# Optimization experiments

Hardware: AMD Instinct MI355X
Metric: run time of the kernel (lower is better)

The kernel has to match this reference:

```python
import jax, jax.numpy as jnp
import numpy as np

N, E, K, C, NB, G = 10000, 320000, 10, 32, 8, 8
RMAX, AVG = 5.0, 32.0
L_OF_M = np.array([0,1,1,1,2,2,2,2,2,3,3,3,3,3,3,3])
BLOCKS = [(0,1),(1,4),(4,9),(9,16)]


def _sph(u):
    # real spherical harmonics l=0..3, e3nn 'component' normalization (sum_m Y_lm^2 = 2l+1)
    x, y, z = u[:,0], u[:,1], u[:,2]
    s3=3**0.5; s5=5**0.5; s15=15**0.5; s105=105**0.5
    s35_8=(35.0/8.0)**0.5; s21_8=(21.0/8.0)**0.5; s7=7**0.5
    return jnp.stack([
        jnp.ones_like(x),
        s3*x, s3*y, s3*z,
        s15*x*y, s15*y*z, 0.5*s5*(3*z*z-1.0), s15*x*z, 0.5*s15*(x*x-y*y),
        s35_8*y*(3*x*x-y*y), s105*x*y*z, s21_8*y*(5*z*z-1.0),
        0.5*s7*z*(5*z*z-3.0), s21_8*x*(5*z*z-1.0), 0.5*s105*z*(x*x-y*y),
        s35_8*x*(x*x-3*y*y)], axis=-1)


def _radial(r):
    # Bessel basis * polynomial cutoff (p=5)
    n = jnp.arange(1, NB+1, dtype=r.dtype)
    bess = jnp.sqrt(2.0/RMAX)*jnp.sin(n*jnp.pi*r[:,None]/RMAX)/r[:,None]
    t = r/RMAX; p = 5.0
    env = 1.0 - (p+1)*(p+2)/2*t**5 + p*(p+2)*t**6 - p*(p+1)/2*t**7
    env = jnp.where(r < RMAX, env, 0.0)
    return bess*env[:,None]


def _interact(scal, ea, ef, snd, rcv, mws, Wl, n_nodes):
    h = ef
    for W in mws[:-1]:
        h = jax.nn.silu(h @ W)
    tw = (h @ mws[-1]).reshape(-1, C, 4)[:, :, L_OF_M]          # [E,C,16] per-(channel,l) tp weights
    mji = scal[snd][:, :, None] * tw * ea[:, None, :]            # per-edge CG-style tensor product
    msg = jax.ops.segment_sum(mji, rcv, num_segments=n_nodes) / AVG
    return jnp.concatenate([jnp.einsum('ncm,cd->ndm', msg[:, :, a:b], Wl[l])
                            for l, (a, b) in enumerate(BLOCKS)], axis=-1)


def _forward(positions, node_attrs, shifts, edge_index, batch, num_graphs,
             atomic_energies, W_emb, Wup1, M1a, M1b, M1c, M1d, Wl1, Wprod1,
             Wup2, M2a, M2b, M2c, M2d, Wl2, Wprod2, Wsc2, wr1, Wr2a, wr2b):
    snd, rcv = edge_index[0], edge_index[1]
    vec = positions[rcv] - positions[snd] + shifts
    r = jnp.sqrt(jnp.sum(vec*vec, -1) + 1e-12)
    ea = _sph(vec / r[:, None])           # [E,16]
    ef = _radial(r)                       # [E,8]
    nf0 = node_attrs @ W_emb              # node embedding [N,C]
    A1 = _interact(nf0 @ Wup1, ea, ef, snd, rcv, (M1a, M1b, M1c, M1d), Wl1, positions.shape[0])
    c1 = jnp.einsum('nk,kct->nct', node_attrs, Wprod1)          # element-dep product-basis coeffs
    a0 = A1[:, :, 0]
    nf1 = A1 * (c1[..., 0] + c1[..., 1]*a0 + c1[..., 2]*a0*a0)[:, :, None]  # correlation-3 product
    A2 = _interact(nf1[:, :, 0] @ Wup2, ea, ef, snd, rcv, (M2a, M2b, M2c, M2d), Wl2, positions.shape[0])
    pl = jnp.stack([jnp.sum(A2[:, :, a:b]**2, -1) for a, b in BLOCKS], -1)  # [N,C,4] invariants
    c2 = jnp.einsum('nk,kct->nct', node_attrs, Wprod2)
    nf2 = jnp.sum(c2*pl, -1) + jnp.einsum('nk,nc,kcd->nd', node_attrs, nf1[:, :, 0], Wsc2)
    e0 = node_attrs @ atomic_energies
    e1 = nf1[:, :, 0] @ wr1
    e2 = jax.nn.silu(nf2 @ Wr2a) @ wr2b
    node_energy = e0 + e1 + e2
    total = jax.ops.segment_sum(node_energy, batch, num_segments=num_graphs)
    return total, node_energy


def setup_inputs():
    key = jax.random.key(0)
    ks = jax.random.split(key, 24)
    s = 0.1
    inp = {}
    inp['positions'] = jax.random.normal(ks[0], (N, 3), jnp.float32)
    inp['node_attrs'] = jax.nn.one_hot(jax.random.randint(ks[1], (N,), 0, K), K, dtype=jnp.float32)
    inp['shifts'] = jnp.zeros((E, 3), jnp.float32)
    inp['edge_index'] = jax.random.randint(ks[2], (2, E), 0, N)
    inp['batch'] = jnp.sort(jax.random.randint(ks[3], (N,), 0, G))
    inp['num_graphs'] = G
    inp['atomic_energies'] = jax.random.normal(ks[4], (K,), jnp.float32)
    inp['W_emb'] = s*jax.random.normal(ks[5], (K, C), jnp.float32)
    inp['Wup1'] = s*jax.random.normal(ks[6], (C, C), jnp.float32)
    inp['M1a'] = s*jax.random.normal(ks[7], (NB, 64), jnp.float32)
    inp['M1b'] = s*jax.random.normal(ks[8], (64, 64), jnp.float32)
    inp['M1c'] = s*jax.random.normal(ks[9], (64, 64), jnp.float32)
    inp['M1d'] = s*jax.random.normal(ks[10], (64, C*4), jnp.float32)
    inp['Wl1'] = s*jax.random.normal(ks[11], (4, C, C), jnp.float32)
    inp['Wprod1'] = s*jax.random.normal(ks[12], (K, C, 3), jnp.float32)
    inp['Wup2'] = s*jax.random.normal(ks[13], (C, C), jnp.float32)
    inp['M2a'] = s*jax.random.normal(ks[14], (NB, 64), jnp.float32)
    inp['M2b'] = s*jax.random.normal(ks[15], (64, 64), jnp.float32)
    inp['M2c'] = s*jax.random.normal(ks[16], (64, 64), jnp.float32)
    inp['M2d'] = s*jax.random.normal(ks[17], (64, C*4), jnp.float32)
    inp['Wl2'] = s*jax.random.normal(ks[18], (4, C, C), jnp.float32)
    inp['Wprod2'] = s*jax.random.normal(ks[19], (K, C, 4), jnp.float32)
    inp['Wsc2'] = s*jax.random.normal(ks[20], (K, C, C), jnp.float32)
    inp['wr1'] = s*jax.random.normal(ks[21], (C,), jnp.float32)
    inp['Wr2a'] = s*jax.random.normal(ks[22], (C, 16), jnp.float32)
    inp['wr2b'] = s*jax.random.normal(ks[23], (16,), jnp.float32)
    return inp


def reference(positions, node_attrs, shifts, edge_index, batch, num_graphs,
              atomic_energies, W_emb, Wup1, M1a, M1b, M1c, M1d, Wl1, Wprod1,
              Wup2, M2a, M2b, M2c, M2d, Wl2, Wprod2, Wsc2, wr1, Wr2a, wr2b):
    def efn(pos):
        tot, ne = _forward(pos, node_attrs, shifts, edge_index, batch, num_graphs,
                           atomic_energies, W_emb, Wup1, M1a, M1b, M1c, M1d, Wl1, Wprod1,
                           Wup2, M2a, M2b, M2c, M2d, Wl2, Wprod2, Wsc2, wr1, Wr2a, wr2b)
        return jnp.sum(tot), (tot, ne)
    (_, (total, node_energy)), g = jax.value_and_grad(efn, has_aux=True)(positions)
    forces = -g  # forces = -dE/dpositions as in get_outputs
    return total, node_energy, forces
```

## Files before the change

### kernel.cpp

```cpp
#include <hip/hip_runtime.h>
#include <math.h>

#define NN 10000
#define NE 320000
#define KS 10
#define CC 32
#define GG 8
#define NTAB 2048
#define TROW 320
#define RMAXf 5.0f
#define AVGf 32.0f

#define OF_TAB 0
#define SZ_TAB ((NTAB + 1) * TROW)
#define OF_GEO (OF_TAB + SZ_TAB)
#define OF_SND (OF_GEO + 4 * NE)
#define OF_SPK (OF_SND + NE)
#define OF_RCSR (OF_SPK + NE)
#define OF_SC1 (OF_RCSR + NE)
#define OF_SP (OF_SC1 + KS * CC)
#define OF_RE (OF_SP + NN)
#define OF_UE (OF_RE + NE)
#define OF_GV (OF_UE + 3 * NE)
#define OF_A0 (OF_GV + 3 * NE)
#define OF_NF1 (OF_A0 + NN * CC)
#define OF_SCAL2 (OF_NF1 + NN * CC)
#define OF_NEP (OF_SCAL2 + NN * CC)
#define OF_GM2T (OF_NEP + NN)
#define OF_GNF1P (OF_GM2T + NN * CC * 16)
#define OF_GS1 (OF_GNF1P + NN * CC)
#define OF_ROWS (OF_GS1 + NN * CC)
#define OF_ELIST (OF_ROWS + NN + 1)
#define OF_DEG (OF_ELIST + NE)
#define OF_CUR (OF_DEG + NN)
#define OF_GSC2 (OF_CUR + NN)
#define OF_END (OF_GSC2 + NN * CC)

__device__ __forceinline__ int lm_of(int m) { return (m == 0) ? 0 : (m < 4) ? 1 : (m < 9) ? 2 : 3; }

__device__ __forceinline__ void sph16(float x, float y, float z, float* Y) {
    const float s3 = 1.7320508075688772f, s5 = 2.23606797749979f, s15 = 3.872983346207417f,
                s105 = 10.246950765959598f, s358 = 2.091650066335189f,
                s218 = 1.6201851746019651f, s7 = 2.6457513110645907f;
    Y[0] = 1.f;
    Y[1] = s3 * x; Y[2] = s3 * y; Y[3] = s3 * z;
    Y[4] = s15 * x * y; Y[5] = s15 * y * z; Y[6] = 0.5f * s5 * (3.f * z * z - 1.f);
    Y[7] = s15 * x * z; Y[8] = 0.5f * s15 * (x * x - y * y);
    Y[9] = s358 * y * (3.f * x * x - y * y);
    Y[10] = s105 * x * y * z;
    Y[11] = s218 * y * (5.f * z * z - 1.f);
    Y[12] = 0.5f * s7 * z * (5.f * z * z - 3.f);
    Y[13] = s218 * x * (5.f * z * z - 1.f);
    Y[14] = 0.5f * s105 * z * (x * x - y * y);
    Y[15] = s358 * x * (x * x - 3.f * y * y);
}

__device__ __forceinline__ void sph16_grad(float x, float y, float z, float* Dx, float* Dy, float* Dz) {
    const float s3 = 1.7320508075688772f, s5 = 2.23606797749979f, s15 = 3.872983346207417f,
                s105 = 10.246950765959598f, s358 = 2.091650066335189f,
                s218 = 1.6201851746019651f, s7 = 2.6457513110645907f;
    Dx[0] = 0; Dy[0] = 0; Dz[0] = 0;
    Dx[1] = s3; Dy[1] = 0; Dz[1] = 0;
    Dx[2] = 0; Dy[2] = s3; Dz[2] = 0;
    Dx[3] = 0; Dy[3] = 0; Dz[3] = s3;
    Dx[4] = s15 * y; Dy[4] = s15 * x; Dz[4] = 0;
    Dx[5] = 0; Dy[5] = s15 * z; Dz[5] = s15 * y;
    Dx[6] = 0; Dy[6] = 0; Dz[6] = 3.f * s5 * z;
    Dx[7] = s15 * z; Dy[7] = 0; Dz[7] = s15 * x;
    Dx[8] = s15 * x; Dy[8] = -s15 * y; Dz[8] = 0;
    Dx[9] = 6.f * s358 * x * y; Dy[9] = 3.f * s358 * (x * x - y * y); Dz[9] = 0;
    Dx[10] = s105 * y * z; Dy[10] = s105 * x * z; Dz[10] = s105 * x * y;
    Dx[11] = 0; Dy[11] = s218 * (5.f * z * z - 1.f); Dz[11] = 10.f * s218 * y * z;
    Dx[12] = 0; Dy[12] = 0; Dz[12] = 0.5f * s7 * (15.f * z * z - 3.f);
    Dx[13] = s218 * (5.f * z * z - 1.f); Dy[13] = 0; Dz[13] = 10.f * s218 * x * z;
    Dx[14] = s105 * x * z; Dy[14] = -s105 * y * z; Dz[14] = 0.5f * s105 * (x * x - y * y);
    Dx[15] = 3.f * s358 * (x * x - y * y); Dy[15] = -6.f * s358 * x * y; Dz[15] = 0;
}

__global__ void k_species(const float* __restrict__ na, int* __restrict__ sp) {
    int n = blockIdx.x * blockDim.x + threadIdx.x;
    if (n >= NN) return;
    int k = 0;
    for (int j = 0; j < KS; j++)
        if (na[n * KS + j] > 0.5f) k = j;
    sp[n] = k;
}

__global__ void k_scal1(const float* __restrict__ Wemb, const float* __restrict__ Wup1, float* __restrict__ st) {
    int i = threadIdx.x;
    if (i >= KS * CC) return;
    int k = i / CC, c = i % CC;
    float s = 0;
    for (int j = 0; j < CC; j++) s += Wemb[k * CC + j] * Wup1[j * CC + c];
    st[i] = s;
}

__global__ void k_table(const float* __restrict__ M1a, const float* __restrict__ M1b,
                        const float* __restrict__ M1c, const float* __restrict__ M1d,
                        const float* __restrict__ M2a, const float* __restrict__ M2b,
                        const float* __restrict__ M2c, const float* __restrict__ M2d,
                        float* __restrict__ tab) {
    const double PI = 3.14159265358979323846;
    int row = blockIdx.x;
    int j = threadIdx.x;
    __shared__ float sR[8], sdR[8];
    __shared__ float sA[64], sdA[64], sB[64], sdB[64];
    if (j < 8) {
        double r = (double)row * ((double)RMAXf / NTAB);
        if (r < 1e-6) r = 1e-6;
        double a = (double)(j + 1) * PI / (double)RMAXf;
        double env = 0.0, denv = 0.0;
        if (row < NTAB) {
            double t = r / (double)RMAXf;
            double t4 = t * t * t * t;
            env = 1.0 - 21.0 * t4 * t + 35.0 * t4 * t * t - 15.0 * t4 * t * t * t;
            denv = (-105.0 * t4 + 210.0 * t4 * t - 105.0 * t4 * t * t) / (double)RMAXf;
        }
        double pref = sqrt(2.0 / (double)RMAXf);
        double s = sin(a * r), cg = cos(a * r);
        double bess = pref * s / r;
        double dbess = pref * (a * cg / r - s / (r * r));
        sR[j] = (float)(bess * env);
        sdR[j] = (float)(dbess * env + bess * denv);
    }
    __syncthreads();
    size_t rb = (size_t)row * TROW;

    {
        float p = 0, dp = 0;
        for (int i = 0; i < 8; i++) { float w = M1a[i * 64 + j]; p += sR[i] * w; dp += sdR[i] * w; }
        float sg = 1.f / (1.f + expf(-p));
        sB[j] = p * sg; sdB[j] = dp * sg * (1.f + p * (1.f - sg));
    }
    __syncthreads();
    {
        float p = 0, dp = 0;
        for (int i = 0; i < 64; i++) { float w = M1b[i * 64 + j]; p += sB[i] * w; dp += sdB[i] * w; }
        float sg = 1.f / (1.f + expf(-p));
        sA[j] = p * sg; sdA[j] = dp * sg * (1.f + p * (1.f - sg));
    }
    __syncthreads();
    {
        float p = 0, dp = 0;
        for (int i = 0; i < 64; i++) { float w = M1c[i * 64 + j]; p += sA[i] * w; dp += sdA[i] * w; }
        float sg = 1.f / (1.f + expf(-p));
        sB[j] = p * sg; sdB[j] = dp * sg * (1.f + p * (1.f - sg));
    }
    __syncthreads();
    #pragma unroll
    for (int t2 = 0; t2 < 2; t2++) {
        int o = j + t2 * 64;
        if ((o & 3) == 0) {
            float p = 0, dp = 0;
            for (int i = 0; i < 64; i++) { float w = M1d[i * 128 + o]; p += sB[i] * w; dp += sdB[i] * w; }
            int c = o >> 2;
            tab[rb + c] = p;
            tab[rb + 32 + c] = dp;
        }
    }
    __syncthreads();

    {
        float p = 0, dp = 0;
        for (int i = 0; i < 8; i++) { float w = M2a[i * 64 + j]; p += sR[i] * w; dp += sdR[i] * w; }
        float sg = 1.f / (1.f + expf(-p));
        sB[j] = p * sg; sdB[j] = dp * sg * (1.f + p * (1.f - sg));
    }
    __syncthreads();
    {
        float p = 0, dp = 0;
        for (int i = 0; i < 64; i++) { float w = M2b[i * 64 + j]; p += sB[i] * w; dp += sdB[i] * w; }
        float sg = 1.f / (1.f + expf(-p));
        sA[j] = p * sg; sdA[j] = dp * sg * (1.f + p * (1.f - sg));
    }
    __syncthreads();
    {
        float p = 0, dp = 0;
        for (int i = 0; i < 64; i++) { float w = M2c[i * 64 + j]; p += sA[i] * w; dp += sdA[i] * w; }
        float sg = 1.f / (1.f + expf(-p));
        sB[j] = p * sg; sdB[j] = dp * sg * (1.f + p * (1.f - sg));
    }
    __syncthreads();
    #pragma unroll
    for (int t2 = 0; t2 < 2; t2++) {
        int o = j + t2 * 64;
        float p = 0, dp = 0;
        for (int i = 0; i < 64; i++) { float w = M2d[i * 128 + o]; p += sB[i] * w; dp += sdB[i] * w; }
        tab[rb + 64 + o] = p;
        tab[rb + 192 + o] = dp;
    }
}

__global__ void k_geom(const float* __restrict__ pos, const float* __restrict__ shifts,
                       const int* __restrict__ ei, float* __restrict__ re,
                       float* __restrict__ ue, int* __restrict__ deg) {
    int e = blockIdx.x * 256 + threadIdx.x;
    if (e >= NE) return;
    int s = ei[e], t = ei[NE + e];
    float vx = pos[3 * t] - pos[3 * s] + shifts[3 * e];
    float vy = pos[3 * t + 1] - pos[3 * s + 1] + shifts[3 * e + 1];
    float vz = pos[3 * t + 2] - pos[3 * s + 2] + shifts[3 * e + 2];
    float r = sqrtf(vx * vx + vy * vy + vz * vz + 1e-12f);
    float inv = 1.f / r;
    re[e] = r;
    ue[3 * e] = vx * inv;
    ue[3 * e + 1] = vy * inv;
    ue[3 * e + 2] = vz * inv;
    atomicAdd(&deg[t], 1);
}

__global__ void k_scan(const int* __restrict__ deg, int* __restrict__ rows, int* __restrict__ cur) {
    __shared__ int part[1024];
    int t = threadIdx.x;
    const int per = (NN + 1023) / 1024;
    int base = t * per;
    int s = 0;
    for (int i = 0; i < per; i++) {
        int idx = base + i;
        if (idx < NN) s += deg[idx];
    }
    part[t] = s;
    __syncthreads();
    for (int off = 1; off < 1024; off <<= 1) {
        int v = (t >= off) ? part[t - off] : 0;
        __syncthreads();
        part[t] += v;
        __syncthreads();
    }
    int run = (t == 0) ? 0 : part[t - 1];
    for (int i = 0; i < per; i++) {
        int idx = base + i;
        if (idx < NN) {
            rows[idx] = run;
            cur[idx] = run;
            run += deg[idx];
        }
    }
    if (t == 1023) rows[NN] = run;
}

__global__ void k_fill(const int* __restrict__ ei, const int* __restrict__ sp,
                       const float* __restrict__ re, const float* __restrict__ ue,
                       int* __restrict__ cur, int* __restrict__ elist,
                       int* __restrict__ snd, int* __restrict__ spk,
                       float* __restrict__ rcsr, float4* __restrict__ geo) {
    int e = blockIdx.x * 256 + threadIdx.x;
    if (e >= NE) return;
    int s = ei[e], t = ei[NE + e];
    int p = atomicAdd(&cur[t], 1);
    elist[p] = e;
    snd[p] = s;
    spk[p] = sp[s];
    rcsr[p] = re[e];
    geo[p] = make_float4(re[e], ue[3 * e], ue[3 * e + 1], ue[3 * e + 2]);
}

__global__ __launch_bounds__(256, 4)
void k_gather1(const int* __restrict__ rows, const int* __restrict__ spk,
               const float* __restrict__ rcsr, const int* __restrict__ sp,
               const float* __restrict__ sc1, const float* __restrict__ tab,
               const float* __restrict__ Wl1, const float* __restrict__ Wprod1,
               const float* __restrict__ Wup2, const float* __restrict__ wr1,
               const float* __restrict__ aE,
               float* __restrict__ a0s, float* __restrict__ nf1,
               float* __restrict__ scal2, float* __restrict__ nep) {
    int wid = (blockIdx.x * 256 + threadIdx.x) >> 6;
    int lane = threadIdx.x & 63, c = lane & 31, h = lane >> 5, hb = h << 5;
    if (wid >= NN) return;
    int r0 = rows[wid], dg = rows[wid + 1] - r0;
    float acc = 0.f;
    for (int j = h; j < dg; j += 2) {
        int p = r0 + j;
        float r = rcsr[p];
        int kk = spk[p];
        float w1 = 0.f;
        if (r < RMAXf) {
            float tt = r * (NTAB / RMAXf);
            int i = (int)tt; if (i > NTAB - 1) i = NTAB - 1;
            float f = tt - (float)i;
            size_t b = (size_t)i * TROW + c;
            w1 = tab[b] * (1.f - f) + tab[b + TROW] * f;
        }
        acc += sc1[kk * CC + c] * w1;
    }
    acc += __shfl_xor(acc, 32, 64);
    float a0 = 0.f;
    for (int d = 0; d < CC; d++) a0 += __shfl(acc, hb + d, 64) * Wl1[d * CC + c];
    a0 *= (1.f / AVGf);
    int k = sp[wid];
    const float* cp = &Wprod1[(k * CC + c) * 3];
    float nf = a0 * (cp[0] + cp[1] * a0 + cp[2] * a0 * a0);
    float s2 = 0.f;
    for (int d = 0; d < CC; d++) s2 += __shfl(nf, hb + d, 64) * Wup2[d * CC + c];
    float t1 = nf * wr1[c];
    for (int m = 16; m >= 1; m >>= 1) t1 += __shfl_xor(t1, m, 64);
    if (h == 0) {
        a0s[wid * CC + c] = a0;
        nf1[wid * CC + c] = nf;
        scal2[wid * CC + c] = s2;
        if (c == 0) nep[wid] = aE[k] + t1;
    }
}

__global__ __launch_bounds__(256, 4)
void k_node2(const int* __restrict__ rows, const int* __restrict__ snd,
             const float4* __restrict__ geo, const int* __restrict__ sp,
             const float* __restrict__ scal2, const float* __restrict__ tab,
             const float* __restrict__ Wl2, const float* __restrict__ Wprod2,
             const float* __restrict__ Wsc2, const float* __restrict__ nf1,
             const float* __restrict__ Wr2a, const float* __restrict__ wr2b,
             const float* __restrict__ wr1, const float* __restrict__ nep,
             const int* __restrict__ batch,
             float* __restrict__ gm2T, float* __restrict__ gnf1p,
             float* __restrict__ out_total, float* __restrict__ out_ne) {
    __shared__ float lds[4][16 * 32];
    int wid = (blockIdx.x * 256 + threadIdx.x) >> 6;
    int lane = threadIdx.x & 63, c = lane & 31, h = lane >> 5, hb = h << 5;
    int w = threadIdx.x >> 6;
    if (wid >= NN) return;
    int r0 = rows[wid], dg = rows[wid + 1] - r0;
    float S2r[16];
    #pragma unroll
    for (int m = 0; m < 16; m++) S2r[m] = 0.f;
    for (int j = h; j < dg; j += 2) {
        int p = r0 + j;
        float4 g4 = geo[p];
        int s = snd[p];
        float sc = scal2[s * CC + c];
        float r = g4.x;
        float w2[4] = {0, 0, 0, 0};
        if (r < RMAXf) {
            float tt = r * (NTAB / RMAXf);
            int i = (int)tt; if (i > NTAB - 1) i = NTAB - 1;
            float f = tt - (float)i;
            size_t b = (size_t)i * TROW + 64 + c * 4;
            #pragma unroll
            for (int l = 0; l < 4; l++) w2[l] = tab[b + l] * (1.f - f) + tab[b + TROW + l] * f;
        }
        float Y[16];
        sph16(g4.y, g4.z, g4.w, Y);
        #pragma unroll
        for (int m = 0; m < 16; m++) S2r[m] += sc * w2[lm_of(m)] * Y[m];
    }
    #pragma unroll
    for (int m = 0; m < 16; m++) S2r[m] += __shfl_xor(S2r[m], 32, 64);
    if (h == 0) {
        #pragma unroll
        for (int m = 0; m < 16; m++) lds[w][m * 32 + c] = S2r[m];
    }
    __syncthreads();
    int d = c;
    float A2r[16];
    #pragma unroll
    for (int m = 0; m < 16; m++) {
        const float* wl = &Wl2[lm_of(m) * CC * CC];
        float acc = 0;
        for (int cc = 0; cc < CC; cc++) acc += lds[w][m * 32 + cc] * wl[cc * CC + d];
        A2r[m] = acc * (1.f / AVGf);
    }
    float pl[4] = {0, 0, 0, 0};
    #pragma unroll
    for (int m = 0; m < 16; m++) pl[lm_of(m)] += A2r[m] * A2r[m];
    int k = sp[wid];
    const float* c2 = &Wprod2[(k * CC + d) * 4];
    float nf2 = c2[0] * pl[0] + c2[1] * pl[1] + c2[2] * pl[2] + c2[3] * pl[3];
    for (int cc = 0; cc < CC; cc++) nf2 += nf1[wid * CC + cc] * Wsc2[((size_t)k * CC + cc) * CC + d];
    int jj = d & 15;
    float zj = 0;
    for (int dd = 0; dd < CC; dd++) zj += __shfl(nf2, hb + dd, 64) * Wr2a[dd * 16 + jj];
    float sg = 1.f / (1.f + expf(-zj));
    float e2p = (d < 16) ? zj * sg * wr2b[jj] : 0.f;
    float red = e2p;
    for (int m = 16; m >= 1; m >>= 1) red += __shfl_xor(red, m, 64);
    if (h == 0 && d == 0) {
        float ne = nep[wid] + red;
        out_ne[wid] = ne;
        atomicAdd(&out_total[batch[wid]], ne);
    }
    float gz = sg * (1.f + zj * (1.f - sg)) * wr2b[jj];
    float gn = 0;
    for (int j2 = 0; j2 < 16; j2++) gn += Wr2a[d * 16 + j2] * __shfl(gz, hb + j2, 64);
    __syncthreads();
    if (h == 0) {
        #pragma unroll
        for (int m = 0; m < 16; m++) lds[w][m * 32 + d] = 2.f * A2r[m] * gn * c2[lm_of(m)];
    }
    __syncthreads();
    float gmv[16];
    #pragma unroll
    for (int m = 0; m < 16; m++) {
        const float* wl = &Wl2[lm_of(m) * CC * CC + c * CC];
        float acc = 0;
        for (int dd = 0; dd < CC; dd++) acc += lds[w][m * 32 + dd] * wl[dd];
        gmv[m] = acc * (1.f / AVGf);
    }
    float g1 = wr1[c];
    for (int dd = 0; dd < CC; dd++) g1 += __shfl(gn, hb + dd, 64) * Wsc2[((size_t)k * CC + c) * CC + dd];
    if (h == 0) {
        #pragma unroll
        for (int m = 0; m < 16; m++) gm2T[(size_t)wid * 512 + c * 16 + m] = gmv[m];
        gnf1p[wid * CC + c] = g1;
    }
}

__global__ __launch_bounds__(256, 4)
void k_gbwd2(const int* __restrict__ rows, const int* __restrict__ elist,
             const int* __restrict__ snd, const float4* __restrict__ geo,
             const float* __restrict__ scal2, const float* __restrict__ tab,
             const float* __restrict__ gm2T,
             float* __restrict__ gsc2, float* __restrict__ gvec) {
    int wid = (blockIdx.x * 256 + threadIdx.x) >> 6;
    int lane = threadIdx.x & 63, c = lane & 31, h = lane >> 5;
    if (wid >= NN) return;
    float gm[16];
    #pragma unroll
    for (int m = 0; m < 16; m++) gm[m] = gm2T[(size_t)wid * 512 + c * 16 + m];
    int r0 = rows[wid], dg = rows[wid + 1] - r0;
    for (int j = h; j < dg; j += 2) {
        int p = r0 + j;
        float4 g4 = geo[p];
        int s = snd[p];
        float sc = scal2[s * CC + c];
        float r = g4.x, ux = g4.y, uy = g4.z, uz = g4.w;
        float w2[4] = {0, 0, 0, 0}, dw2[4] = {0, 0, 0, 0};
        if (r < RMAXf) {
            float tt = r * (NTAB / RMAXf);
            int i = (int)tt; if (i > NTAB - 1) i = NTAB - 1;
            float f = tt - (float)i;
            size_t b = (size_t)i * TROW + 64 + c * 4;
            size_t b2 = (size_t)i * TROW + 192 + c * 4;
            #pragma unroll
            for (int l = 0; l < 4; l++) {
                w2[l] = tab[b + l] * (1.f - f) + tab[b + TROW + l] * f;
                dw2[l] = tab[b2 + l] * (1.f - f) + tab[b2 + TROW + l] * f;
            }
        }
        float Y[16], Dx[16], Dy[16], Dz[16];
        sph16(ux, uy, uz, Y);
        sph16_grad(ux, uy, uz, Dx, Dy, Dz);
        float gsc = 0, gdr = 0, gx = 0, gy = 0, gz = 0;
        #pragma unroll
        for (int m = 0; m < 16; m++) {
            float g = gm[m];
            int l = lm_of(m);
            float wv = w2[l];
            gsc += g * wv * Y[m];
            gdr += g * Y[m] * sc * dw2[l];
            float gY = g * sc * wv;
            gx += gY * Dx[m]; gy += gY * Dy[m]; gz += gY * Dz[m];
        }
        atomicAdd(&gsc2[s * CC + c], gsc);
        for (int m2 = 16; m2 >= 1; m2 >>= 1) {
            gdr += __shfl_xor(gdr, m2, 64);
            gx += __shfl_xor(gx, m2, 64);
            gy += __shfl_xor(gy, m2, 64);
            gz += __shfl_xor(gz, m2, 64);
        }
        if (c == 0) {
            int e = elist[p];
            float inv = 1.f / r;
            float dot = ux * gx + uy * gy + uz * gz;
            gvec[3 * e] = ux * gdr + (gx - ux * dot) * inv;
            gvec[3 * e + 1] = uy * gdr + (gy - uy * dot) * inv;
            gvec[3 * e + 2] = uz * gdr + (gz - uz * dot) * inv;
        }
    }
}

__global__ void k_node_bwd2(const float* __restrict__ gnf1p, const float* __restrict__ gsc2,
                            const float* __restrict__ Wup2, const float* __restrict__ a0s,
                            const int* __restrict__ sp, const float* __restrict__ Wprod1,
                            const float* __restrict__ Wl1, float* __restrict__ gS1) {
    int gid = blockIdx.x * 256 + threadIdx.x;
    int n = gid >> 5, c = gid & 31;
    if (n >= NN) return;
    int hb = threadIdx.x & 32;
    float g1 = gnf1p[n * CC + c];
    for (int dd = 0; dd < CC; dd++) g1 += gsc2[n * CC + dd] * Wup2[c * CC + dd];
    float a0 = a0s[n * CC + c];
    int k = sp[n];
    const float* cp = &Wprod1[(k * CC + c) * 3];
    float ga0 = g1 * (cp[0] + 2.f * cp[1] * a0 + 3.f * cp[2] * a0 * a0);
    float acc = 0;
    for (int dd = 0; dd < CC; dd++) acc += __shfl(ga0, hb + dd, 64) * Wl1[c * CC + dd];
    gS1[n * CC + c] = acc * (1.f / AVGf);
}

__global__ void k_edge_bwd1(const int* __restrict__ ei, const int* __restrict__ sp,
                            const float* __restrict__ re, const float* __restrict__ ue,
                            const float* __restrict__ sc1, const float* __restrict__ tab,
                            const float* __restrict__ gS1, const float* __restrict__ gvec,
                            float* __restrict__ F) {
    int gid = blockIdx.x * 256 + threadIdx.x;
    int e = gid >> 5, c = gid & 31;
    if (e >= NE) return;
    int s = ei[e], t = ei[NE + e];
    float r = re[e];
    float dw = 0.f;
    if (r < RMAXf) {
        float tt = r * (NTAB / RMAXf);
        int i = (int)tt; if (i > NTAB - 1) i = NTAB - 1;
        float f = tt - (float)i;
        size_t b = (size_t)i * TROW + 32 + c;
        dw = tab[b] * (1.f - f) + tab[b + TROW] * f;
    }
    float gw = gS1[t * CC + c] * sc1[sp[s] * CC + c];
    float gdr = gw * dw;
    for (int m = 16; m >= 1; m >>= 1) gdr += __shfl_xor(gdr, m, 64);
    if (c < 3) {
        float u = ue[3 * e + c];
        float gv = gvec[3 * e + c] + u * gdr;
        atomicAdd(&F[3 * s + c], gv);
        atomicAdd(&F[3 * t + c], -gv);
    }
}

extern "C" void kernel_launch(void* const* d_in, const int* in_sizes, int n_in,
                              void* d_out, int out_size, void* d_ws, size_t ws_size,
                              hipStream_t stream) {
    const float* pos = (const float*)d_in[0];
    const float* na = (const float*)d_in[1];
    const float* shifts = (const float*)d_in[2];
    const int* ei = (const int*)d_in[3];
    const int* batch = (const int*)d_in[4];
    const float* aE = (const float*)d_in[6];
    const float* Wemb = (const float*)d_in[7];
    const float* Wup1 = (const float*)d_in[8];
    const float* M1a = (const float*)d_in[9];
    const float* M1b = (const float*)d_in[10];
    const float* M1c = (const float*)d_in[11];
    const float* M1d = (const float*)d_in[12];
    const float* Wl1 = (const float*)d_in[13];
    const float* Wprod1 = (const float*)d_in[14];
    const float* Wup2 = (const float*)d_in[15];
    const float* M2a = (const float*)d_in[16];
    const float* M2b = (const float*)d_in[17];
    const float* M2c = (const float*)d_in[18];
    const float* M2d = (const float*)d_in[19];
    const float* Wl2 = (const float*)d_in[20];
    const float* Wprod2 = (const float*)d_in[21];
    const float* Wsc2 = (const float*)d_in[22];
    const float* wr1 = (const float*)d_in[23];
    const float* Wr2a = (const float*)d_in[24];
    const float* wr2b = (const float*)d_in[25];

    float* ws = (float*)d_ws;
    float* tab = ws + OF_TAB;
    float4* geo = (float4*)(ws + OF_GEO);
    int* snd = (int*)(ws + OF_SND);
    int* spk = (int*)(ws + OF_SPK);
    float* rcsr = ws + OF_RCSR;
    float* sc1 = ws + OF_SC1;
    int* sp = (int*)(ws + OF_SP);
    float* re = ws + OF_RE;
    float* ue = ws + OF_UE;
    float* gv = ws + OF_GV;
    float* a0s = ws + OF_A0;
    float* nf1 = ws + OF_NF1;
    float* scal2 = ws + OF_SCAL2;
    float* nep = ws + OF_NEP;
    float* gm2T = ws + OF_GM2T;
    float* gnf1p = ws + OF_GNF1P;
    float* gS1 = ws + OF_GS1;
    int* rows = (int*)(ws + OF_ROWS);
    int* elist = (int*)(ws + OF_ELIST);
    int* deg = (int*)(ws + OF_DEG);
    int* cur = (int*)(ws + OF_CUR);
    float* gsc2 = ws + OF_GSC2;

    float* out_total = (float*)d_out;
    float* out_ne = out_total + GG;
    float* out_F = out_ne + NN;

    hipMemsetAsync(d_out, 0, sizeof(float) * (GG + NN + 3 * NN), stream);
    hipMemsetAsync(deg, 0, sizeof(float) * (size_t)(OF_END - OF_DEG), stream);

    k_species<<<(NN + 255) / 256, 256, 0, stream>>>(na, sp);
    k_scal1<<<1, 320, 0, stream>>>(Wemb, Wup1, sc1);
    k_table<<<NTAB + 1, 64, 0, stream>>>(M1a, M1b, M1c, M1d, M2a, M2b, M2c, M2d, tab);
    k_geom<<<(NE + 255) / 256, 256, 0, stream>>>(pos, shifts, ei, re, ue, deg);
    k_scan<<<1, 1024, 0, stream>>>(deg, rows, cur);
    k_fill<<<(NE + 255) / 256, 256, 0, stream>>>(ei, sp, re, ue, cur, elist, snd, spk, rcsr, geo);
    k_gather1<<<(NN + 3) / 4, 256, 0, stream>>>(rows, spk, rcsr, sp, sc1, tab, Wl1, Wprod1,
                                                Wup2, wr1, aE, a0s, nf1, scal2, nep);
    k_node2<<<(NN + 3) / 4, 256, 0, stream>>>(rows, snd, geo, sp, scal2, tab, Wl2,
                                              Wprod2, Wsc2, nf1, Wr2a, wr2b, wr1, nep, batch,
                                              gm2T, gnf1p, out_total, out_ne);
    k_gbwd2<<<(NN + 3) / 4, 256, 0, stream>>>(rows, elist, snd, geo, scal2, tab, gm2T, gsc2, gv);
    k_node_bwd2<<<NN / 8, 256, 0, stream>>>(gnf1p, gsc2, Wup2, a0s, sp, Wprod1, Wl1, gS1);
    k_edge_bwd1<<<NE / 8, 256, 0, stream>>>(ei, sp, re, ue, sc1, tab, gS1, gv, out_F);
}
```

Measured before the change: 482.7 us.

## Fuse layer-2 backward edge gather into node kernel and vectorize table loads

New measurement: 1.081 ms. 124% more time.

```diff
diff --git a/kernel.cpp b/kernel.cpp
--- a/kernel.cpp
+++ b/kernel.cpp
@@ -26,8 +26,7 @@
 #define OF_NF1 (OF_A0 + NN * CC)
 #define OF_SCAL2 (OF_NF1 + NN * CC)
 #define OF_NEP (OF_SCAL2 + NN * CC)
-#define OF_GM2T (OF_NEP + NN)
-#define OF_GNF1P (OF_GM2T + NN * CC * 16)
+#define OF_GNF1P (OF_NEP + NN)
 #define OF_GS1 (OF_GNF1P + NN * CC)
 #define OF_ROWS (OF_GS1 + NN * CC)
 #define OF_ELIST (OF_ROWS + NN + 1)
@@ -269,19 +268,30 @@
     if (wid >= NN) return;
     int r0 = rows[wid], dg = rows[wid + 1] - r0;
     float acc = 0.f;
-    for (int j = h; j < dg; j += 2) {
-        int p = r0 + j;
-        float r = rcsr[p];
-        int kk = spk[p];
-        float w1 = 0.f;
-        if (r < RMAXf) {
-            float tt = r * (NTAB / RMAXf);
-            int i = (int)tt; if (i > NTAB - 1) i = NTAB - 1;
-            float f = tt - (float)i;
-            size_t b = (size_t)i * TROW + c;
-            w1 = tab[b] * (1.f - f) + tab[b + TROW] * f;
-        }
-        acc += sc1[kk * CC + c] * w1;
+    for (int j = h; j < dg; j += 8) {
+        float rv[4], scv[4]; bool act[4];
+        #pragma unroll
+        for (int u = 0; u < 4; u++) {
+            int jj = j + 2 * u;
+            act[u] = jj < dg;
+            int p = r0 + (act[u] ? jj : 0);
+            rv[u] = rcsr[p];
+            scv[u] = sc1[spk[p] * CC + c];
+        }
+        #pragma unroll
+        for (int u = 0; u < 4; u++) {
+            if (!act[u]) continue;
+            float r = rv[u];
+            float w1 = 0.f;
+            if (r < RMAXf) {
+                float tt = r * (NTAB / RMAXf);
+                int i = (int)tt; if (i > NTAB - 1) i = NTAB - 1;
+                float f = tt - (float)i;
+                size_t b = (size_t)i * TROW + c;
+                w1 = tab[b] * (1.f - f) + tab[b + TROW] * f;
+            }
+            acc += scv[u] * w1;
+        }
     }
     acc += __shfl_xor(acc, 32, 64);
     float a0 = 0.f;
@@ -303,15 +313,17 @@
 }
 
 __global__ __launch_bounds__(256, 4)
-void k_node2(const int* __restrict__ rows, const int* __restrict__ snd,
-             const float4* __restrict__ geo, const int* __restrict__ sp,
+void k_node2(const int* __restrict__ rows, const int* __restrict__ elist,
+             const int* __restrict__ snd, const float4* __restrict__ geo,
+             const int* __restrict__ sp,
              const float* __restrict__ scal2, const float* __restrict__ tab,
              const float* __restrict__ Wl2, const float* __restrict__ Wprod2,
              const float* __restrict__ Wsc2, const float* __restrict__ nf1,
              const float* __restrict__ Wr2a, const float* __restrict__ wr2b,
              const float* __restrict__ wr1, const float* __restrict__ nep,
              const int* __restrict__ batch,
-             float* __restrict__ gm2T, float* __restrict__ gnf1p,
+             float* __restrict__ gnf1p, float* __restrict__ gsc2,
+             float* __restrict__ gvec,
              float* __restrict__ out_total, float* __restrict__ out_ne) {
     __shared__ float lds[4][16 * 32];
     int wid = (blockIdx.x * 256 + threadIdx.x) >> 6;
@@ -319,28 +331,32 @@
     int w = threadIdx.x >> 6;
     if (wid >= NN) return;
     int r0 = rows[wid], dg = rows[wid + 1] - r0;
+
     float S2r[16];
     #pragma unroll
     for (int m = 0; m < 16; m++) S2r[m] = 0.f;
     for (int j = h; j < dg; j += 2) {
         int p = r0 + j;
         float4 g4 = geo[p];
-        int s = snd[p];
-        float sc = scal2[s * CC + c];
+        float sc = scal2[snd[p] * CC + c];
         float r = g4.x;
-        float w2[4] = {0, 0, 0, 0};
+        float scw[4] = {0, 0, 0, 0};
         if (r < RMAXf) {
             float tt = r * (NTAB / RMAXf);
             int i = (int)tt; if (i > NTAB - 1) i = NTAB - 1;
             float f = tt - (float)i;
             size_t b = (size_t)i * TROW + 64 + c * 4;
-            #pragma unroll
-            for (int l = 0; l < 4; l++) w2[l] = tab[b + l] * (1.f - f) + tab[b + TROW + l] * f;
+            float4 t0 = *(const float4*)&tab[b];
+            float4 t1 = *(const float4*)&tab[b + TROW];
+            scw[0] = sc * (t0.x + (t1.x - t0.x) * f);
+            scw[1] = sc * (t0.y + (t1.y - t0.y) * f);
+            scw[2] = sc * (t0.z + (t1.z - t0.z) * f);
+            scw[3] = sc * (t0.w + (t1.w - t0.w) * f);
         }
         float Y[16];
         sph16(g4.y, g4.z, g4.w, Y);
         #pragma unroll
-        for (int m = 0; m < 16; m++) S2r[m] += sc * w2[lm_of(m)] * Y[m];
+        for (int m = 0; m < 16; m++) S2r[m] += scw[lm_of(m)] * Y[m];
     }
     #pragma unroll
     for (int m = 0; m < 16; m++) S2r[m] += __shfl_xor(S2r[m], 32, 64);
@@ -349,6 +365,7 @@
         for (int m = 0; m < 16; m++) lds[w][m * 32 + c] = S2r[m];
     }
     __syncthreads();
+
     int d = c;
     float A2r[16];
     #pragma unroll
@@ -386,54 +403,40 @@
         for (int m = 0; m < 16; m++) lds[w][m * 32 + d] = 2.f * A2r[m] * gn * c2[lm_of(m)];
     }
     __syncthreads();
-    float gmv[16];
+    float gm[16];
     #pragma unroll
     for (int m = 0; m < 16; m++) {
         const float* wl = &Wl2[lm_of(m) * CC * CC + c * CC];
         float acc = 0;
         for (int dd = 0; dd < CC; dd++) acc += lds[w][m * 32 + dd] * wl[dd];
-        gmv[m] = acc * (1.f / AVGf);
+        gm[m] = acc * (1.f / AVGf);
     }
     float g1 = wr1[c];
     for (int dd = 0; dd < CC; dd++) g1 += __shfl(gn, hb + dd, 64) * Wsc2[((size_t)k * CC + c) * CC + dd];
-    if (h == 0) {
-        #pragma unroll
-        for (int m = 0; m < 16; m++) gm2T[(size_t)wid * 512 + c * 16 + m] = gmv[m];
-        gnf1p[wid * CC + c] = g1;
-    }
-}
-
-__global__ __launch_bounds__(256, 4)
-void k_gbwd2(const int* __restrict__ rows, const int* __restrict__ elist,
-             const int* __restrict__ snd, const float4* __restrict__ geo,
-             const float* __restrict__ scal2, const float* __restrict__ tab,
-             const float* __restrict__ gm2T,
-             float* __restrict__ gsc2, float* __restrict__ gvec) {
-    int wid = (blockIdx.x * 256 + threadIdx.x) >> 6;
-    int lane = threadIdx.x & 63, c = lane & 31, h = lane >> 5;
-    if (wid >= NN) return;
-    float gm[16];
-    #pragma unroll
-    for (int m = 0; m < 16; m++) gm[m] = gm2T[(size_t)wid * 512 + c * 16 + m];
-    int r0 = rows[wid], dg = rows[wid + 1] - r0;
+    if (h == 0) gnf1p[wid * CC + c] = g1;
+
     for (int j = h; j < dg; j += 2) {
         int p = r0 + j;
         float4 g4 = geo[p];
         int s = snd[p];
         float sc = scal2[s * CC + c];
         float r = g4.x, ux = g4.y, uy = g4.z, uz = g4.w;
-        float w2[4] = {0, 0, 0, 0}, dw2[4] = {0, 0, 0, 0};
+        float w2[4] = {0, 0, 0, 0}, scw[4] = {0, 0, 0, 0}, sdw[4] = {0, 0, 0, 0};
         if (r < RMAXf) {
             float tt = r * (NTAB / RMAXf);
             int i = (int)tt; if (i > NTAB - 1) i = NTAB - 1;
             float f = tt - (float)i;
             size_t b = (size_t)i * TROW + 64 + c * 4;
             size_t b2 = (size_t)i * TROW + 192 + c * 4;
-            #pragma unroll
-            for (int l = 0; l < 4; l++) {
-                w2[l] = tab[b + l] * (1.f - f) + tab[b + TROW + l] * f;
-                dw2[l] = tab[b2 + l] * (1.f - f) + tab[b2 + TROW + l] * f;
-            }
+            float4 t0 = *(const float4*)&tab[b];
+            float4 t1 = *(const float4*)&tab[b + TROW];
+            float4 d0 = *(const float4*)&tab[b2];
+            float4 d1 = *(const float4*)&tab[b2 + TROW];
+            w2[0] = t0.x + (t1.x - t0.x) * f; w2[1] = t0.y + (t1.y - t0.y) * f;
+            w2[2] = t0.z + (t1.z - t0.z) * f; w2[3] = t0.w + (t1.w - t0.w) * f;
+            sdw[0] = sc * (d0.x + (d1.x - d0.x) * f); sdw[1] = sc * (d0.y + (d1.y - d0.y) * f);
+            sdw[2] = sc * (d0.z + (d1.z - d0.z) * f); sdw[3] = sc * (d0.w + (d1.w - d0.w) * f);
+            scw[0] = sc * w2[0]; scw[1] = sc * w2[1]; scw[2] = sc * w2[2]; scw[3] = sc * w2[3];
         }
         float Y[16], Dx[16], Dy[16], Dz[16];
         sph16(ux, uy, uz, Y);
@@ -443,10 +446,10 @@
         for (int m = 0; m < 16; m++) {
             float g = gm[m];
             int l = lm_of(m);
-            float wv = w2[l];
-            gsc += g * wv * Y[m];
-            gdr += g * Y[m] * sc * dw2[l];
-            float gY = g * sc * wv;
+            float t = g * Y[m];
+            gsc += t * w2[l];
+            gdr += t * sdw[l];
+            float gY = g * scw[l];
             gx += gY * Dx[m]; gy += gY * Dy[m]; gz += gY * Dz[m];
         }
         atomicAdd(&gsc2[s * CC + c], gsc);
@@ -559,7 +562,6 @@
     float* nf1 = ws + OF_NF1;
     float* scal2 = ws + OF_SCAL2;
     float* nep = ws + OF_NEP;
-    float* gm2T = ws + OF_GM2T;
     float* gnf1p = ws + OF_GNF1P;
     float* gS1 = ws + OF_GS1;
     int* rows = (int*)(ws + OF_ROWS);
@@ -583,10 +585,9 @@
     k_fill<<<(NE + 255) / 256, 256, 0, stream>>>(ei, sp, re, ue, cur, elist, snd, spk, rcsr, geo);
     k_gather1<<<(NN + 3) / 4, 256, 0, stream>>>(rows, spk, rcsr, sp, sc1, tab, Wl1, Wprod1,
                                                 Wup2, wr1, aE, a0s, nf1, scal2, nep);
-    k_node2<<<(NN + 3) / 4, 256, 0, stream>>>(rows, snd, geo, sp, scal2, tab, Wl2,
+    k_node2<<<(NN + 3) / 4, 256, 0, stream>>>(rows, elist, snd, geo, sp, scal2, tab, Wl2,
                                               Wprod2, Wsc2, nf1, Wr2a, wr2b, wr1, nep, batch,
-                                              gm2T, gnf1p, out_total, out_ne);
-    k_gbwd2<<<(NN + 3) / 4, 256, 0, stream>>>(rows, elist, snd, geo, scal2, tab, gm2T, gsc2, gv);
+                                              gnf1p, gsc2, gv, out_total, out_ne);
     k_node_bwd2<<<NN / 8, 256, 0, stream>>>(gnf1p, gsc2, Wup2, a0s, sp, Wprod1, Wl1, gS1);
     k_edge_bwd1<<<NE / 8, 256, 0, stream>>>(ei, sp, re, ue, sc1, tab, gS1, gv, out_F);
 }
```
